# Performance work log

Hardware: AMD Instinct MI355X
Metric: run time of the kernel (lower is better)

Reference implementation:

```python
import jax, jax.numpy as jnp
import numpy as np

N = 100000   # num_nodes
E = 1600000  # num_edges (avg degree 16)
F = 128      # input features
U = 128      # units


def setup_inputs() -> dict:
    key = jax.random.key(0)
    k1, k2, k3, k4 = jax.random.split(key, 4)
    x = jax.random.normal(k1, (N, F), dtype=jnp.float32)
    edge_index = jax.random.randint(k2, (2, E), 0, N, dtype=jnp.int32)
    edge_weight = jax.random.uniform(k3, (E,), dtype=jnp.float32)
    glorot = (2.0 / (F + U)) ** 0.5
    kernel = jax.random.normal(k4, (F, U), dtype=jnp.float32) * glorot
    bias = jnp.zeros((U,), dtype=jnp.float32)
    return {"x": x, "edge_index": edge_index, "edge_weight": edge_weight,
            "kernel": kernel, "bias": bias}


def reference(x, edge_index, edge_weight, kernel, bias):
    num_nodes = x.shape[0]
    row, col = edge_index[0], edge_index[1]
    # renorm trick: A' = A + I (self-loop weight = 1.0 since improved=False)
    loop_idx = jnp.arange(num_nodes, dtype=edge_index.dtype)
    row = jnp.concatenate([row, loop_idx])
    col = jnp.concatenate([col, loop_idx])
    w = jnp.concatenate([edge_weight, jnp.ones((num_nodes,), dtype=edge_weight.dtype)])
    # symmetric normalization: D^{-1/2} A' D^{-1/2}; sym=True -> degrees = row sums
    deg = jax.ops.segment_sum(w, row, num_segments=num_nodes)
    dinv = jnp.where(deg > 0, jax.lax.rsqrt(deg), 0.0)
    w_norm = dinv[row] * w * dinv[col]
    # dense transform then sparse propagate: out[row] += w_norm * (XW)[col]
    h = x @ kernel                              # [N, U]
    msg = w_norm[:, None] * h[col]              # [E+N, U]
    out = jax.ops.segment_sum(msg, row, num_segments=num_nodes)  # [N, U]
    return jax.nn.relu(out + bias)
```

## Files before the change

### kernel.cpp

```cpp
#include <hip/hip_runtime.h>
#include <math.h>


#define CAP 48
#define BINSZ 128
#define NBLK 2048

typedef __attribute__((ext_vector_type(8))) short bf16x8;
typedef __attribute__((ext_vector_type(4))) float f32x4;

__device__ __forceinline__ ushort f2bf(float f) {
  uint u = __float_as_uint(f);
  return (ushort)((u + 0x7FFFu + ((u >> 16) & 1u)) >> 16);
}


__global__ __launch_bounds__(256) void k_hist(
    const int* __restrict__ row, uint* __restrict__ histT, int E, int nbins) {
  __shared__ uint h[1024];
  int tid = threadIdx.x;
  for (int t = tid; t < nbins; t += 256) h[t] = 0;
  __syncthreads();
  int per = (E + NBLK - 1) / NBLK;
  int e0 = blockIdx.x * per;
  int e1 = min(e0 + per, E);
  for (int e = e0 + tid; e < e1; e += 256)
    atomicAdd(&h[(uint)row[e] >> 7], 1u);
  __syncthreads();
  for (int t = tid; t < nbins; t += 256)
    histT[(size_t)t * NBLK + blockIdx.x] = h[t];
}

__global__ __launch_bounds__(256) void k_scanA(uint* __restrict__ histT,
                                               uint* __restrict__ bintot) {
  __shared__ uint ts[256];
  int t = threadIdx.x;
  uint* rowp = histT + (size_t)blockIdx.x * NBLK;
  uint loc[8];
  uint s = 0;
#pragma unroll
  for (int i = 0; i < 8; ++i) { loc[i] = rowp[t * 8 + i]; s += loc[i]; }
  ts[t] = s;
  __syncthreads();
  for (int d = 1; d < 256; d <<= 1) {
    uint add = (t >= d) ? ts[t - d] : 0;
    __syncthreads();
    ts[t] += add;
    __syncthreads();
  }
  if (t == 255) bintot[blockIdx.x] = ts[255];
  uint run = ts[t] - s;
#pragma unroll
  for (int i = 0; i < 8; ++i) { uint v = loc[i]; rowp[t * 8 + i] = run; run += v; }
}

__global__ void k_scanB(const uint* __restrict__ bintot,
                        uint* __restrict__ binbase, int nbins) {
  __shared__ uint s[1024];
  int t = threadIdx.x;
  uint v = (t < nbins) ? bintot[t] : 0;
  s[t] = v;
  __syncthreads();
  for (int d = 1; d < 1024; d <<= 1) {
    uint add = (t >= d) ? s[t - d] : 0;
    __syncthreads();
    s[t] += add;
    __syncthreads();
  }
  if (t < nbins) {
    binbase[t] = s[t] - v;
    if (t == nbins - 1) binbase[nbins] = s[t];
  }
}

__global__ __launch_bounds__(256) void k_scatter2(
    const int* __restrict__ row, const int* __restrict__ col,
    const float* __restrict__ ew, const uint* __restrict__ histT,
    const uint* __restrict__ binbase, int2* __restrict__ binned,
    int E, int nbins) {
  __shared__ uint sbase[1024];
  int tid = threadIdx.x;
  for (int t = tid; t < nbins; t += 256)
    sbase[t] = binbase[t] + histT[(size_t)t * NBLK + blockIdx.x];
  __syncthreads();
  int per = (E + NBLK - 1) / NBLK;
  int e0 = blockIdx.x * per;
  int e1 = min(e0 + per, E);
  for (int e = e0 + tid; e < e1; e += 256) {
    int r = row[e];
    int bin = (uint)r >> 7;
    uint pos = atomicAdd(&sbase[bin], 1u);
    uint wq = (uint)__float2int_rn(ew[e] * 32768.0f);
    if (wq > 32767u) wq = 32767u;
    int2 v;
    v.x = (int)(((uint)col[e] & 0x1FFFFu) | (wq << 17));
    v.y = r & (BINSZ - 1);
    binned[pos] = v;
  }
}

__global__ __launch_bounds__(256) void k_binbuild(
    const int2* __restrict__ binned, const uint* __restrict__ binbase,
    uint* __restrict__ slot, int* __restrict__ cnt, float* __restrict__ dinv,
    int N) {
  __shared__ uint sl[BINSZ * CAP];
  __shared__ uint scnt[BINSZ];
  int bin = blockIdx.x;
  int tid = threadIdx.x;
  if (tid < BINSZ) scnt[tid] = 0;
  __syncthreads();
  uint start = binbase[bin];
  uint ec = binbase[bin + 1] - start;
  const int2* src = binned + start;
  for (uint i = tid; i < ec; i += 256) {
    int2 v = src[i];
    uint ro = (uint)v.y;
    uint pos = atomicAdd(&scnt[ro], 1u);
    if (pos < (uint)CAP) sl[ro * CAP + pos] = (uint)v.x;
  }
  __syncthreads();
  int node = bin * BINSZ + tid;
  if (tid < BINSZ && node < N) {
    uint c = min(scnt[tid], (uint)CAP);
    float s = 0.0f;
    for (uint p = 0; p < c; ++p) s += (float)(sl[tid * CAP + p] >> 17);
    dinv[node] = 1.0f / sqrtf(fmaf(s, 1.0f / 32768.0f, 1.0f));
    cnt[node] = (int)c;
  }
  uint4* dst = (uint4*)(slot + (size_t)bin * BINSZ * CAP);
  const uint4* s4 = (const uint4*)sl;
#pragma unroll
  for (int it = 0; it < (BINSZ * CAP) / (4 * 256); ++it)
    dst[it * 256 + tid] = s4[it * 256 + tid];
}

__global__ __launch_bounds__(256) void k_gemm3(const float* __restrict__ x,
                                               const float* __restrict__ W,
                                               ushort* __restrict__ hb, int N) {
  __shared__ ushort Wl[16384];
  int tid = threadIdx.x;
  {
    const float4* Wv = (const float4*)W;
#pragma unroll
    for (int it = 0; it < 16; ++it) {
      int id4 = it * 256 + tid;
      float4 v = Wv[id4];
      int id = id4 * 4;
      int k = id >> 7;
      int n = id & 127;
      int kb = k >> 3, klo = k & 7;
      Wl[(n + 0) * 128 + (((kb ^ ((n + 0) & 7)) << 3) | klo)] = f2bf(v.x);
      Wl[(n + 1) * 128 + (((kb ^ ((n + 1) & 7)) << 3) | klo)] = f2bf(v.y);
      Wl[(n + 2) * 128 + (((kb ^ ((n + 2) & 7)) << 3) | klo)] = f2bf(v.z);
      Wl[(n + 3) * 128 + (((kb ^ ((n + 3) & 7)) << 3) | klo)] = f2bf(v.w);
    }
  }
  __syncthreads();

  int wave = tid >> 6, lane = tid & 63;
  int g = lane >> 4;
  int m = lane & 15;

  int ntiles = (N + 63) >> 6;
  for (int tile = blockIdx.x; tile < ntiles; tile += gridDim.x) {
    int r0 = tile * 64 + wave * 16;
    int row = r0 + m;
    bool ok = row < N;
    const float* xr = x + (size_t)row * 128;

    bf16x8 afr[4];
#pragma unroll
    for (int kt = 0; kt < 4; ++kt) {
      float4 p0, p1;
      if (ok) {
        p0 = *(const float4*)(xr + kt * 32 + g * 8);
        p1 = *(const float4*)(xr + kt * 32 + g * 8 + 4);
      } else {
        p0 = make_float4(0.f, 0.f, 0.f, 0.f);
        p1 = p0;
      }
      afr[kt][0] = (short)f2bf(p0.x); afr[kt][1] = (short)f2bf(p0.y);
      afr[kt][2] = (short)f2bf(p0.z); afr[kt][3] = (short)f2bf(p0.w);
      afr[kt][4] = (short)f2bf(p1.x); afr[kt][5] = (short)f2bf(p1.y);
      afr[kt][6] = (short)f2bf(p1.z); afr[kt][7] = (short)f2bf(p1.w);
    }

#pragma unroll
    for (int nt = 0; nt < 8; ++nt) {
      int n = nt * 16 + m;
      f32x4 acc = {0.f, 0.f, 0.f, 0.f};
#pragma unroll
      for (int kt = 0; kt < 4; ++kt) {
        int kb = (kt * 4 + g) ^ (n & 7);
        bf16x8 b = *(const bf16x8*)&Wl[n * 128 + kb * 8];
        acc = __builtin_amdgcn_mfma_f32_16x16x32_bf16(afr[kt], b, acc, 0, 0, 0);
      }
#pragma unroll
      for (int r = 0; r < 4; ++r) {
        int orow = r0 + g * 4 + r;
        if (orow < N) hb[(size_t)orow * 128 + nt * 16 + m] = f2bf(acc[r]);
      }
    }
  }
}

__global__ __launch_bounds__(256) void k_agg2(
    const ushort* __restrict__ hb, const int* __restrict__ cnt,
    const uint* __restrict__ slot, const float* __restrict__ dinv,
    const float* __restrict__ bias, float* __restrict__ out, int n0, int n1) {
  int wid = n0 + blockIdx.x * 4 + (threadIdx.x >> 6);
  int lane = threadIdx.x & 63;
  if (wid >= n1) return;
  float di = dinv[wid];
  uint hv = *(const uint*)(hb + (size_t)wid * 128 + lane * 2);
  float ax = di * __uint_as_float(hv << 16);
  float ay = di * __uint_as_float(hv & 0xFFFF0000u);
  int e = min(cnt[wid], CAP);
  const uint* sl = slot + (size_t)wid * CAP;
  int p = 0;
  for (; p + 4 <= e; p += 4) {
    uint s0 = sl[p], s1 = sl[p + 1], s2 = sl[p + 2], s3 = sl[p + 3];
    int c0 = s0 & 0x1FFFF, c1 = s1 & 0x1FFFF, c2 = s2 & 0x1FFFF, c3 = s3 & 0x1FFFF;
    float w0 = (float)(s0 >> 17) * (1.0f / 32768.0f) * dinv[c0];
    float w1 = (float)(s1 >> 17) * (1.0f / 32768.0f) * dinv[c1];
    float w2 = (float)(s2 >> 17) * (1.0f / 32768.0f) * dinv[c2];
    float w3 = (float)(s3 >> 17) * (1.0f / 32768.0f) * dinv[c3];
    uint g0 = *(const uint*)(hb + (size_t)c0 * 128 + lane * 2);
    uint g1 = *(const uint*)(hb + (size_t)c1 * 128 + lane * 2);
    uint g2 = *(const uint*)(hb + (size_t)c2 * 128 + lane * 2);
    uint g3 = *(const uint*)(hb + (size_t)c3 * 128 + lane * 2);
    ax = fmaf(w0, __uint_as_float(g0 << 16), ax);
    ay = fmaf(w0, __uint_as_float(g0 & 0xFFFF0000u), ay);
    ax = fmaf(w1, __uint_as_float(g1 << 16), ax);
    ay = fmaf(w1, __uint_as_float(g1 & 0xFFFF0000u), ay);
    ax = fmaf(w2, __uint_as_float(g2 << 16), ax);
    ay = fmaf(w2, __uint_as_float(g2 & 0xFFFF0000u), ay);
    ax = fmaf(w3, __uint_as_float(g3 << 16), ax);
    ay = fmaf(w3, __uint_as_float(g3 & 0xFFFF0000u), ay);
  }
  for (; p < e; ++p) {
    uint s = sl[p];
    int c = s & 0x1FFFF;
    float w = (float)(s >> 17) * (1.0f / 32768.0f) * dinv[c];
    uint gg = *(const uint*)(hb + (size_t)c * 128 + lane * 2);
    ax = fmaf(w, __uint_as_float(gg << 16), ax);
    ay = fmaf(w, __uint_as_float(gg & 0xFFFF0000u), ay);
  }
  float2 bv = *(const float2*)(bias + lane * 2);
  float2 o;
  o.x = fmaxf(fmaf(di, ax, bv.x), 0.0f);
  o.y = fmaxf(fmaf(di, ay, bv.y), 0.0f);
  *(float2*)(out + (size_t)wid * 128 + lane * 2) = o;
}


__global__ void k_deg_cnt(const int* __restrict__ row, const float* __restrict__ ew,
                          float* __restrict__ degF, int* __restrict__ cnt, int E) {
  int idx = blockIdx.x * blockDim.x + threadIdx.x;
  int stride = gridDim.x * blockDim.x;
  for (int e = idx; e < E; e += stride) {
    int r = row[e];
    atomicAdd(&degF[r], ew[e]);
    atomicAdd(&cnt[r], 1);
  }
}

__global__ void k_dinv(float* degF, int N) {
  int i = blockIdx.x * blockDim.x + threadIdx.x;
  if (i < N) degF[i] = 1.0f / sqrtf(degF[i] + 1.0f);
}

__global__ void k_scan1(const int* __restrict__ cnt, int* __restrict__ bsum, int N) {
  __shared__ int s[256];
  int i = blockIdx.x * 256 + threadIdx.x;
  s[threadIdx.x] = (i < N) ? cnt[i] : 0;
  __syncthreads();
  for (int d = 128; d > 0; d >>= 1) {
    if (threadIdx.x < d) s[threadIdx.x] += s[threadIdx.x + d];
    __syncthreads();
  }
  if (threadIdx.x == 0) bsum[blockIdx.x] = s[0];
}

__global__ void k_scan2(const int* __restrict__ bsum, int* __restrict__ bsx, int NB) {
  __shared__ int s[1024];
  int t = threadIdx.x;
  int v = (t < NB) ? bsum[t] : 0;
  s[t] = v;
  __syncthreads();
  for (int d = 1; d < 1024; d <<= 1) {
    int add = (t >= d) ? s[t - d] : 0;
    __syncthreads();
    s[t] += add;
    __syncthreads();
  }
  if (t < NB) bsx[t] = s[t] - v;
}

__global__ void k_scan3(const int* __restrict__ cnt, const int* __restrict__ bsx,
                        int* __restrict__ offs, int* __restrict__ cur, int N) {
  __shared__ int s[256];
  int t = threadIdx.x;
  int i = blockIdx.x * 256 + t;
  int v = (i < N) ? cnt[i] : 0;
  s[t] = v;
  __syncthreads();
  for (int d = 1; d < 256; d <<= 1) {
    int add = (t >= d) ? s[t - d] : 0;
    __syncthreads();
    s[t] += add;
    __syncthreads();
  }
  if (i < N) {
    int excl = bsx[blockIdx.x] + s[t] - v;
    offs[i] = excl;
    cur[i] = excl;
  }
}

__global__ void k_scatter(const int* __restrict__ row, const int* __restrict__ col,
                          const float* __restrict__ ew, const float* __restrict__ dinv,
                          int* __restrict__ cur, int* __restrict__ ccol,
                          float* __restrict__ cw, int E) {
  int idx = blockIdx.x * blockDim.x + threadIdx.x;
  int stride = gridDim.x * blockDim.x;
  for (int e = idx; e < E; e += stride) {
    int r = row[e], c = col[e];
    int pos = atomicAdd(&cur[r], 1);
    ccol[pos] = c;
    cw[pos] = dinv[r] * ew[e] * dinv[c];
  }
}

__global__ __launch_bounds__(256) void k_gemm(const float* __restrict__ x,
                                              const float* __restrict__ W,
                                              float* __restrict__ h, int N) {
  __shared__ float Ks[64][128];
  __shared__ float xs[64][36];
  int tid = threadIdx.x;
  int cg = tid & 31;
  int rg = tid >> 5;
  int ntiles = (N + 31) >> 5;
  for (int tile = blockIdx.x; tile < ntiles; tile += gridDim.x) {
    int r0 = tile << 5;
    float acc[4][4] = {};
    for (int kt = 0; kt < 2; ++kt) {
      {
        const float4* Wv = (const float4*)(W + kt * 64 * 128);
        float4* Kv = (float4*)&Ks[0][0];
#pragma unroll
        for (int q = 0; q < 8; ++q) Kv[q * 256 + tid] = Wv[q * 256 + tid];
      }
      {
        int r = tid >> 3;
        int c0 = (tid & 7) * 8;
        int grow = r0 + r;
        if (grow < N) {
          const float4* xp = (const float4*)(x + (size_t)grow * 128 + kt * 64 + c0);
          float4 a = xp[0], b = xp[1];
          xs[c0 + 0][r] = a.x; xs[c0 + 1][r] = a.y; xs[c0 + 2][r] = a.z; xs[c0 + 3][r] = a.w;
          xs[c0 + 4][r] = b.x; xs[c0 + 5][r] = b.y; xs[c0 + 6][r] = b.z; xs[c0 + 7][r] = b.w;
        } else {
#pragma unroll
          for (int q = 0; q < 8; ++q) xs[c0 + q][r] = 0.0f;
        }
      }
      __syncthreads();
#pragma unroll 8
      for (int k = 0; k < 64; ++k) {
        float4 a = *(const float4*)&xs[k][rg * 4];
        float4 b = *(const float4*)&Ks[k][cg * 4];
        float av[4] = {a.x, a.y, a.z, a.w};
        float bv[4] = {b.x, b.y, b.z, b.w};
#pragma unroll
        for (int rr = 0; rr < 4; ++rr)
#pragma unroll
          for (int cc = 0; cc < 4; ++cc)
            acc[rr][cc] = fmaf(av[rr], bv[cc], acc[rr][cc]);
      }
      __syncthreads();
    }
#pragma unroll
    for (int rr = 0; rr < 4; ++rr) {
      int grow = r0 + rg * 4 + rr;
      if (grow < N) {
        float4 v = make_float4(acc[rr][0], acc[rr][1], acc[rr][2], acc[rr][3]);
        *(float4*)&h[(size_t)grow * 128 + cg * 4] = v;
      }
    }
  }
}

__global__ __launch_bounds__(256) void k_agg(
    const float* __restrict__ h, const int* __restrict__ offs,
    const int* __restrict__ cnt, const int* __restrict__ ccol,
    const float* __restrict__ cw, const float* __restrict__ dinv,
    const float* __restrict__ bias, float* __restrict__ out, int N) {
  int wid = blockIdx.x * (blockDim.x >> 6) + (threadIdx.x >> 6);
  int lane = threadIdx.x & 63;
  if (wid >= N) return;
  float di = dinv[wid];
  float2 hv = *(const float2*)(h + (size_t)wid * 128 + lane * 2);
  float ax = di * di * hv.x;
  float ay = di * di * hv.y;
  int s = offs[wid];
  int e = s + cnt[wid];
  int p = s;
  for (; p + 4 <= e; p += 4) {
    int c0 = ccol[p], c1 = ccol[p + 1], c2 = ccol[p + 2], c3 = ccol[p + 3];
    float w0 = cw[p], w1 = cw[p + 1], w2 = cw[p + 2], w3 = cw[p + 3];
    float2 h0 = *(const float2*)(h + (size_t)c0 * 128 + lane * 2);
    float2 h1 = *(const float2*)(h + (size_t)c1 * 128 + lane * 2);
    float2 h2 = *(const float2*)(h + (size_t)c2 * 128 + lane * 2);
    float2 h3 = *(const float2*)(h + (size_t)c3 * 128 + lane * 2);
    ax = fmaf(w0, h0.x, ax); ay = fmaf(w0, h0.y, ay);
    ax = fmaf(w1, h1.x, ax); ay = fmaf(w1, h1.y, ay);
    ax = fmaf(w2, h2.x, ax); ay = fmaf(w2, h2.y, ay);
    ax = fmaf(w3, h3.x, ax); ay = fmaf(w3, h3.y, ay);
  }
  for (; p < e; ++p) {
    int c = ccol[p];
    float w = cw[p];
    float2 hh = *(const float2*)(h + (size_t)c * 128 + lane * 2);
    ax = fmaf(w, hh.x, ax); ay = fmaf(w, hh.y, ay);
  }
  float2 bv = *(const float2*)(bias + lane * 2);
  float2 o;
  o.x = fmaxf(ax + bv.x, 0.0f);
  o.y = fmaxf(ay + bv.y, 0.0f);
  *(float2*)(out + (size_t)wid * 128 + lane * 2) = o;
}


extern "C" void kernel_launch(void* const* d_in, const int* in_sizes, int n_in,
                              void* d_out, int out_size, void* d_ws, size_t ws_size,
                              hipStream_t stream) {
  const float* x    = (const float*)d_in[0];
  const int*   ei   = (const int*)d_in[1];
  const float* ew   = (const float*)d_in[2];
  const float* W    = (const float*)d_in[3];
  const float* bias = (const float*)d_in[4];
  int N = in_sizes[0] / 128;
  int E = in_sizes[2];
  const int* row = ei;
  const int* col = ei + E;

  char* ws = (char*)d_ws;
  size_t ofs = 0;
  auto alloc = [&](size_t bytes) -> void* {
    void* p = ws + ofs;
    ofs += (bytes + 255) & ~(size_t)255;
    return p;
  };

  int nbins = (N + BINSZ - 1) / BINSZ;

  size_t need_fast = (((size_t)N * 256 + 255) & ~(size_t)255)
                   + (((size_t)nbins * BINSZ * CAP * 4 + 255) & ~(size_t)255)
                   + (((size_t)E * 8 + 255) & ~(size_t)255)
                   + (((size_t)nbins * NBLK * 4 + 255) & ~(size_t)255)
                   + 2 * (((size_t)N * 4 + 255) & ~(size_t)255)
                   + 16384;

  bool shapes_ok = (N <= 131072) && (in_sizes[0] == N * 128) &&
                   (in_sizes[3] == 128 * 128) && (in_sizes[4] == 128);

  int nb = (N + 255) / 256;

  if (shapes_ok && ws_size >= need_fast) {
    ushort* hb      = (ushort*)alloc((size_t)N * 256);
    uint*   slot    = (uint*)  alloc((size_t)nbins * BINSZ * CAP * 4);
    int2*   binned  = (int2*)  alloc((size_t)E * 8);
    uint*   histT   = (uint*)  alloc((size_t)nbins * NBLK * 4);
    int*    cnt     = (int*)   alloc((size_t)N * 4);
    float*  dinv    = (float*) alloc((size_t)N * 4);
    uint*   bintot  = (uint*)  alloc(8192);
    uint*   binbase = (uint*)  alloc(8192);

    k_gemm3<<<1024, 256, 0, stream>>>(x, W, hb, N);
    k_hist<<<NBLK, 256, 0, stream>>>(row, histT, E, nbins);
    k_scanA<<<nbins, 256, 0, stream>>>(histT, bintot);
    k_scanB<<<1, 1024, 0, stream>>>(bintot, binbase, nbins);
    k_scatter2<<<NBLK, 256, 0, stream>>>(row, col, ew, histT, binbase, binned,
                                         E, nbins);
    k_binbuild<<<nbins, 256, 0, stream>>>(binned, binbase, slot, cnt, dinv, N);

    int nh = (N + 1) / 2;
    int g1 = (nh + 3) / 4;
    int g2 = (N - nh + 3) / 4;
    k_agg2<<<g1, 256, 0, stream>>>(hb, cnt, slot, dinv, bias, (float*)d_out, 0, nh);
    k_agg2<<<g2, 256, 0, stream>>>(hb, cnt, slot, dinv, bias, (float*)d_out, nh, N);
  } else {
    float* h    = (float*)alloc((size_t)N * 512);
    float* degF = (float*)alloc((size_t)N * 4);
    int*   cntF = (int*)  alloc((size_t)N * 4);
    int*   offs = (int*)  alloc((size_t)N * 4);
    int*   cur  = (int*)  alloc((size_t)N * 4);
    int*   bsum = (int*)  alloc(4096 * 4);
    int*   bsx  = (int*)  alloc(4096 * 4);
    int*   ccol = (int*)  alloc((size_t)E * 4);
    float* cw   = (float*)alloc((size_t)E * 4);

    hipMemsetAsync(degF, 0, (size_t)N * 4, stream);
    hipMemsetAsync(cntF, 0, (size_t)N * 4, stream);

    k_gemm<<<1024, 256, 0, stream>>>(x, W, h, N);
    k_deg_cnt<<<2048, 256, 0, stream>>>(row, ew, degF, cntF, E);
    k_dinv<<<nb, 256, 0, stream>>>(degF, N);
    k_scan1<<<nb, 256, 0, stream>>>(cntF, bsum, N);
    k_scan2<<<1, 1024, 0, stream>>>(bsum, bsx, nb);
    k_scan3<<<nb, 256, 0, stream>>>(cntF, bsx, offs, cur, N);
    k_scatter<<<2048, 256, 0, stream>>>(row, col, ew, degF, cur, ccol, cw, E);
    int nodeBlocks = (N + 3) / 4;
    k_agg<<<nodeBlocks, 256, 0, stream>>>(h, offs, cntF, ccol, cw, degF, bias,
                                          (float*)d_out, N);
  }
}
```

Baseline: 275.9 us.

## Stage GEMM tiles through LDS for coalesced loads and vectorized bf16 stores

The persistent grid-stride GEMM kernel becomes one 64-row tile per block, launched as two half grids. Each tile's x rows are loaded with coalesced float4 reads into a padded LDS buffer as bf16, and MFMA fragments are read from LDS. Results are staged back through LDS so the bf16 output is written with 16-byte row-contiguous stores instead of scattered 2-byte writes. The cost is that every block now reloads and converts the full W matrix into LDS for a single tile, and the extra LDS use lowers occupancy.

```diff
diff --git a/kernel.cpp b/kernel.cpp
--- a/kernel.cpp
+++ b/kernel.cpp
@@ -5,8 +5,10 @@
 #define CAP 48
 #define BINSZ 128
 #define NBLK 2048
+#define XST 136
 
 typedef __attribute__((ext_vector_type(8))) short bf16x8;
+typedef __attribute__((ext_vector_type(8))) ushort ushort8;
 typedef __attribute__((ext_vector_type(4))) float f32x4;
 
 __device__ __forceinline__ ushort f2bf(float f) {
@@ -134,10 +136,12 @@
     dst[it * 256 + tid] = s4[it * 256 + tid];
 }
 
-__global__ __launch_bounds__(256) void k_gemm3(const float* __restrict__ x,
+__global__ __launch_bounds__(256) void k_gemm4(const float* __restrict__ x,
                                                const float* __restrict__ W,
-                                               ushort* __restrict__ hb, int N) {
+                                               ushort* __restrict__ hb,
+                                               int N, int tile0) {
   __shared__ ushort Wl[16384];
+  __shared__ ushort xl[64 * XST];
   int tid = threadIdx.x;
   {
     const float4* Wv = (const float4*)W;
@@ -155,52 +159,61 @@
       Wl[(n + 3) * 128 + (((kb ^ ((n + 3) & 7)) << 3) | klo)] = f2bf(v.w);
     }
   }
+
+  int r0 = (tile0 + blockIdx.x) * 64;
+  {
+#pragma unroll
+    for (int it = 0; it < 8; ++it) {
+      int id4 = it * 256 + tid;
+      int el = id4 * 4;
+      int row = el >> 7;
+      int colc = el & 127;
+      int grow = r0 + row;
+      float4 v = make_float4(0.f, 0.f, 0.f, 0.f);
+      if (grow < N) v = *(const float4*)(x + (size_t)grow * 128 + colc);
+      ushort* dst = &xl[row * XST + colc];
+      dst[0] = f2bf(v.x); dst[1] = f2bf(v.y);
+      dst[2] = f2bf(v.z); dst[3] = f2bf(v.w);
+    }
+  }
   __syncthreads();
 
   int wave = tid >> 6, lane = tid & 63;
   int g = lane >> 4;
   int m = lane & 15;
 
-  int ntiles = (N + 63) >> 6;
-  for (int tile = blockIdx.x; tile < ntiles; tile += gridDim.x) {
-    int r0 = tile * 64 + wave * 16;
-    int row = r0 + m;
-    bool ok = row < N;
-    const float* xr = x + (size_t)row * 128;
-
-    bf16x8 afr[4];
+  bf16x8 afr[4];
+#pragma unroll
+  for (int kt = 0; kt < 4; ++kt)
+    afr[kt] = *(const bf16x8*)&xl[(wave * 16 + m) * XST + kt * 32 + g * 8];
+
+  f32x4 acc[8] = {};
+#pragma unroll
+  for (int nt = 0; nt < 8; ++nt) {
+    int n = nt * 16 + m;
 #pragma unroll
     for (int kt = 0; kt < 4; ++kt) {
-      float4 p0, p1;
-      if (ok) {
-        p0 = *(const float4*)(xr + kt * 32 + g * 8);
-        p1 = *(const float4*)(xr + kt * 32 + g * 8 + 4);
-      } else {
-        p0 = make_float4(0.f, 0.f, 0.f, 0.f);
-        p1 = p0;
-      }
-      afr[kt][0] = (short)f2bf(p0.x); afr[kt][1] = (short)f2bf(p0.y);
-      afr[kt][2] = (short)f2bf(p0.z); afr[kt][3] = (short)f2bf(p0.w);
-      afr[kt][4] = (short)f2bf(p1.x); afr[kt][5] = (short)f2bf(p1.y);
-      afr[kt][6] = (short)f2bf(p1.z); afr[kt][7] = (short)f2bf(p1.w);
+      int kb = (kt * 4 + g) ^ (n & 7);
+      bf16x8 b = *(const bf16x8*)&Wl[n * 128 + kb * 8];
+      acc[nt] = __builtin_amdgcn_mfma_f32_16x16x32_bf16(afr[kt], b, acc[nt], 0, 0, 0);
     }
-
-#pragma unroll
-    for (int nt = 0; nt < 8; ++nt) {
-      int n = nt * 16 + m;
-      f32x4 acc = {0.f, 0.f, 0.f, 0.f};
-#pragma unroll
-      for (int kt = 0; kt < 4; ++kt) {
-        int kb = (kt * 4 + g) ^ (n & 7);
-        bf16x8 b = *(const bf16x8*)&Wl[n * 128 + kb * 8];
-        acc = __builtin_amdgcn_mfma_f32_16x16x32_bf16(afr[kt], b, acc, 0, 0, 0);
-      }
-#pragma unroll
-      for (int r = 0; r < 4; ++r) {
-        int orow = r0 + g * 4 + r;
-        if (orow < N) hb[(size_t)orow * 128 + nt * 16 + m] = f2bf(acc[r]);
-      }
-    }
+  }
+
+#pragma unroll
+  for (int nt = 0; nt < 8; ++nt)
+#pragma unroll
+    for (int r = 0; r < 4; ++r)
+      xl[(wave * 16 + g * 4 + r) * XST + nt * 16 + m] = f2bf(acc[nt][r]);
+  __syncthreads();
+
+#pragma unroll
+  for (int it = 0; it < 4; ++it) {
+    int c = it * 256 + tid;
+    int row = c >> 4, cc = c & 15;
+    int grow = r0 + row;
+    if (grow < N)
+      *(ushort8*)&hb[(size_t)grow * 128 + cc * 8] =
+          *(const ushort8*)&xl[row * XST + cc * 8];
   }
 }
 
@@ -477,7 +490,11 @@
     uint*   bintot  = (uint*)  alloc(8192);
     uint*   binbase = (uint*)  alloc(8192);
 
-    k_gemm3<<<1024, 256, 0, stream>>>(x, W, hb, N);
+    int T = (N + 63) / 64;
+    int T1 = T / 2;
+    k_gemm4<<<T1, 256, 0, stream>>>(x, W, hb, N, 0);
+    k_gemm4<<<T - T1, 256, 0, stream>>>(x, W, hb, N, T1);
+
     k_hist<<<NBLK, 256, 0, stream>>>(row, histT, E, nbins);
     k_scanA<<<nbins, 256, 0, stream>>>(histT, bintot);
     k_scanB<<<1, 1024, 0, stream>>>(bintot, binbase, nbins);
```

Result: slower. 294.0 us (+6.6%).
